# Optimization experiments

Hardware: AMD Instinct MI355X
Metric: run time of the kernel (lower is better)

The kernel has to match this reference:

```python
import jax, jax.numpy as jnp
import numpy as np

B, N, D, E = 2, 50000, 128, 640000


def setup_inputs() -> dict:
    key = jax.random.key(0)
    ks = jax.random.split(key, 7)
    x = jax.random.normal(ks[0], (B, N, D), dtype=jnp.float32)
    edge_index = jax.random.randint(ks[1], (2, E), 0, N)
    edge_attr = jax.random.uniform(ks[2], (E,), dtype=jnp.float32)
    s = 1.0 / np.sqrt(D)
    W1 = jax.random.uniform(ks[3], (D, D), jnp.float32, -s, s)
    b1 = jax.random.uniform(ks[4], (D,), jnp.float32, -s, s)
    W2 = jax.random.uniform(ks[5], (D, D), jnp.float32, -s, s)
    b2 = jax.random.uniform(ks[6], (D,), jnp.float32, -s, s)
    return {"x": x, "edge_index": edge_index, "edge_attr": edge_attr,
            "W1": W1, "b1": b1, "W2": W2, "b2": b2}


def _gcn_layer(x, W, b, row, col, norm, n):
    # x: [B, N, D] -> transform then gather-scale-scatter along edges
    h = jnp.einsum('bnd,df->bnf', x, W)
    msg = h[:, row, :] * norm[None, :, None]          # [B, E2, D]
    agg = jax.vmap(lambda m: jax.ops.segment_sum(m, col, num_segments=n))(msg)
    return agg + b


def reference(x, edge_index, edge_attr, W1, b1, W2, b2):
    n = x.shape[1]
    row, col = edge_index[0], edge_index[1]
    # GCNConv default: add self loops (weight 1), symmetric normalization
    loop = jnp.arange(n)
    row2 = jnp.concatenate([row, loop])
    col2 = jnp.concatenate([col, loop])
    w2 = jnp.concatenate([edge_attr, jnp.ones((n,), edge_attr.dtype)])
    deg = jax.ops.segment_sum(w2, col2, num_segments=n)
    dinv = jnp.where(deg > 0, jax.lax.rsqrt(deg), 0.0)
    norm = dinv[row2] * w2 * dinv[col2]               # [E2]
    # dropout is identity in eval mode
    h = jax.nn.relu(_gcn_layer(x, W1, b1, row2, col2, norm, n))
    h = jax.nn.relu(_gcn_layer(h, W2, b2, row2, col2, norm, n))
    return h
```

## Files before the change

### kernel.cpp

```cpp
#include <hip/hip_runtime.h>

#define NNODES 50000
#define NBATCH 2
#define DIM    128
#define NEDGE  640000
#define M_TOT  (NBATCH*NNODES)
#define NXCD   8
#define NBL_N  196

typedef unsigned short u16;
typedef unsigned int   u32;
typedef unsigned long long u64;

typedef __attribute__((ext_vector_type(8))) short bf16x8;
typedef __attribute__((ext_vector_type(4))) float f32x4;

__device__ __forceinline__ float bf2f(u16 u){ return __uint_as_float(((u32)u)<<16); }
__device__ __forceinline__ u16 f2bf(float f){
    u32 x = __float_as_uint(f);
    x += 0x7fffu + ((x>>16)&1u);
    return (u16)(x>>16);
}

__global__ __launch_bounds__(256) void count_k(const int* __restrict__ ei,
                                               const float* __restrict__ ea,
                                               u64* __restrict__ part,
                                               u32* __restrict__ rankpack){
    u32 xcc = __builtin_amdgcn_s_getreg(6164) & 7u;
    int e = blockIdx.x*256 + threadIdx.x;
    if (e < NEDGE){
        int c = ei[NEDGE + e];
        u64 inc = (((u64)__float2uint_rn(ea[e] * 16777216.0f)) << 32) | 1ull;
        u64 old = __hip_atomic_fetch_add(&part[(size_t)xcc*NNODES + c], inc,
                                         __ATOMIC_RELAXED, __HIP_MEMORY_SCOPE_WORKGROUP);
        rankpack[e] = ((u32)old & 0xffffu) | (xcc << 16);
    }
}

__global__ __launch_bounds__(256) void scan1(const u64* __restrict__ part,
                                             int* __restrict__ cnt,
                                             int* __restrict__ poff,
                                             float* __restrict__ dinv,
                                             int* colstart, int* bsum){
    __shared__ int s[256];
    int tid = threadIdx.x;
    int n = blockIdx.x*256 + tid;
    int v = 0;
    if (n < NNODES){
        int run = 0; u64 fsum = 0;
        #pragma unroll
        for (int p = 0; p < NXCD; ++p){
            u64 pv = part[(size_t)p*NNODES + n];
            poff[p*NNODES + n] = run;
            run  += (int)(pv & 0xffffffffu);
            fsum += (pv >> 32);
        }
        cnt[n] = run;
        v = run;
        float deg = 1.0f + (float)fsum * (1.0f/16777216.0f);
        dinv[n] = rsqrtf(deg);
    }
    s[tid] = v; __syncthreads();
    #pragma unroll
    for (int off = 1; off < 256; off <<= 1){
        int t = (tid >= off) ? s[tid-off] : 0;
        __syncthreads();
        s[tid] += t;
        __syncthreads();
    }
    if (n < NNODES) colstart[n] = s[tid] - v;
    if (tid == 255) bsum[blockIdx.x] = s[255];
}

__global__ __launch_bounds__(256) void fill_k(const int* __restrict__ ei,
                                              const float* __restrict__ ea,
                                              const float* __restrict__ dinv,
                                              const int* __restrict__ colstart,
                                              const int* __restrict__ bsum,
                                              const int* __restrict__ poff,
                                              const u32* __restrict__ rankpack,
                                              int* __restrict__ colstartF,
                                              u32* __restrict__ epk){
    __shared__ int s[256];
    __shared__ int pre[256];
    int tid = threadIdx.x;
    int v = (tid < NBL_N) ? bsum[tid] : 0;
    s[tid] = v; __syncthreads();
    #pragma unroll
    for (int off = 1; off < 256; off <<= 1){
        int t = (tid >= off) ? s[tid-off] : 0;
        __syncthreads();
        s[tid] += t;
        __syncthreads();
    }
    pre[tid] = s[tid] - v;
    __syncthreads();

    int e = blockIdx.x*256 + tid;
    if (e < NEDGE){
        int r = ei[e], c = ei[NEDGE + e];
        u32 rp = rankpack[e];
        int base = colstart[c] + pre[c >> 8];
        colstartF[c] = base;
        int pos = base + poff[(rp >> 16)*NNODES + c] + (int)(rp & 0xffffu);
        float w = dinv[r] * ea[e] * dinv[c];
        epk[pos] = (u32)r | ((u32)f2bf(w) << 16);
    }
}

__global__ __launch_bounds__(256) void transposeW(const float* __restrict__ W1, u16* __restrict__ Wt1,
                                                  const float* __restrict__ W2, u16* __restrict__ Wt2,
                                                  u64* __restrict__ part){
    int i = blockIdx.x*256 + threadIdx.x;
    const float* W = (i < 16384) ? W1 : W2;
    u16* Wt       = (i < 16384) ? Wt1 : Wt2;
    int ii = i & 16383;
    int k = ii >> 7, n = ii & 127;
    Wt[n*DIM + k] = f2bf(W[ii]);
    for (int z = i; z < NXCD*NNODES; z += 32768) part[z] = 0;
}

__device__ __forceinline__ bf16x8 load_frag(const float* A, size_t off){
    const float4* ap = (const float4*)(A + off);
    float4 lo = ap[0], hi = ap[1];
    bf16x8 r;
    r[0] = (short)f2bf(lo.x); r[1] = (short)f2bf(lo.y);
    r[2] = (short)f2bf(lo.z); r[3] = (short)f2bf(lo.w);
    r[4] = (short)f2bf(hi.x); r[5] = (short)f2bf(hi.y);
    r[6] = (short)f2bf(hi.z); r[7] = (short)f2bf(hi.w);
    return r;
}
__device__ __forceinline__ bf16x8 load_frag(const u16* A, size_t off){
    return *(const bf16x8*)(A + off);
}

template <typename AT, bool PERM>
__global__ __launch_bounds__(256) void gemm128(const AT* __restrict__ A,
                                               const u16* __restrict__ Wt,
                                               u16* __restrict__ H, int M){
    __shared__ u16 Wl[128][136];
    int tid = threadIdx.x;
    {
        const uint4* src = (const uint4*)Wt;
        #pragma unroll
        for (int j = 0; j < 8; ++j){
            int g = tid + j*256;
            int n = g >> 4;
            int k = (g & 15) * 8;
            *(uint4*)&Wl[n][k] = src[g];
        }
    }
    __syncthreads();

    int wave = tid >> 6, lane = tid & 63;
    int quad = lane >> 4, r = lane & 15;
    int row0 = blockIdx.x*256 + wave*64;

    f32x4 acc[4][8];
    #pragma unroll
    for (int mt = 0; mt < 4; ++mt)
        #pragma unroll
        for (int nt = 0; nt < 8; ++nt)
            acc[mt][nt] = (f32x4){0.f,0.f,0.f,0.f};

    #pragma unroll
    for (int ks = 0; ks < 4; ++ks){
        bf16x8 af[4];
        #pragma unroll
        for (int mt = 0; mt < 4; ++mt){
            int row = row0 + mt*16 + r;
            if (row < M)
                af[mt] = load_frag(A, (size_t)row*DIM + ks*32 + quad*8);
            else
                af[mt] = (bf16x8){0,0,0,0,0,0,0,0};
        }
        #pragma unroll
        for (int nt = 0; nt < 8; ++nt){
            bf16x8 bfr = *(const bf16x8*)&Wl[nt*16 + r][ks*32 + quad*8];
            #pragma unroll
            for (int mt = 0; mt < 4; ++mt)
                acc[mt][nt] = __builtin_amdgcn_mfma_f32_16x16x32_bf16(af[mt], bfr, acc[mt][nt], 0, 0, 0);
        }
    }

    #pragma unroll
    for (int mt = 0; mt < 4; ++mt){
        #pragma unroll
        for (int reg = 0; reg < 4; ++reg){
            int row = row0 + mt*16 + quad*4 + reg;
            if (row < M){
                size_t hrow;
                if (PERM){
                    int b = (row >= NNODES);
                    int n = row - b*NNODES;
                    hrow = (size_t)(2*n + b);
                } else {
                    hrow = (size_t)row;
                }
                #pragma unroll
                for (int nt = 0; nt < 8; ++nt)
                    H[hrow*DIM + nt*16 + r] = f2bf(acc[mt][nt][reg]);
            }
        }
    }
}

template <bool OUT_F32>
__global__ __launch_bounds__(256) void gather6_k(const u16* __restrict__ Hi,
                                                 const u32* __restrict__ epk,
                                                 const int* __restrict__ colstartF,
                                                 const int* __restrict__ cnt,
                                                 const float* __restrict__ dinv,
                                                 const float* __restrict__ bias,
                                                 void* __restrict__ out){
    int wave = threadIdx.x >> 6, lane = threadIdx.x & 63;
    int n = blockIdx.x*4 + wave;
    if (n >= NNODES) return;
    const char* Hb = (const char*)Hi;

    float a0, a1, a2, a3;
    {
        uint2 sv = *(const uint2*)(Hb + (size_t)n*512 + lane*8);
        float dn = dinv[n], dn2 = dn*dn;
        a0 = dn2*__uint_as_float(sv.x << 16);
        a1 = dn2*__uint_as_float(sv.x & 0xffff0000u);
        a2 = dn2*__uint_as_float(sv.y << 16);
        a3 = dn2*__uint_as_float(sv.y & 0xffff0000u);
    }

    int s = colstartF[n], c = cnt[n];
    for (int base = 0; base < c; base += 64){
        int m = min(64, c - base);
        u32 em = 0;
        if (lane < m) em = epk[s + base + lane];
        for (int j = 0; j < m; j += 8){
            #pragma unroll
            for (int g = 0; g < 8; ++g){
                u32 me = __shfl(em, j + g);
                uint2 v = *(const uint2*)(Hb + (size_t)(me & 0xffffu)*512 + lane*8);
                float w = __uint_as_float(me & 0xffff0000u);
                a0 = fmaf(w, __uint_as_float(v.x << 16), a0);
                a1 = fmaf(w, __uint_as_float(v.x & 0xffff0000u), a1);
                a2 = fmaf(w, __uint_as_float(v.y << 16), a2);
                a3 = fmaf(w, __uint_as_float(v.y & 0xffff0000u), a3);
            }
        }
    }

    int sub = lane & 31, b = lane >> 5;
    float4 bb = ((const float4*)bias)[sub];
    a0 = fmaxf(a0 + bb.x, 0.f);
    a1 = fmaxf(a1 + bb.y, 0.f);
    a2 = fmaxf(a2 + bb.z, 0.f);
    a3 = fmaxf(a3 + bb.w, 0.f);
    if (OUT_F32){
        float* O = (float*)out + ((size_t)b*NNODES + n)*DIM + sub*4;
        *(float4*)O = make_float4(a0, a1, a2, a3);
    } else {
        char* O = (char*)out + (size_t)n*512 + lane*8;
        uint2 pk;
        pk.x = (u32)f2bf(a0) | ((u32)f2bf(a1) << 16);
        pk.y = (u32)f2bf(a2) | ((u32)f2bf(a3) << 16);
        *(uint2*)O = pk;
    }
}

extern "C" void kernel_launch(void* const* d_in, const int* in_sizes, int n_in,
                              void* d_out, int out_size, void* d_ws, size_t ws_size,
                              hipStream_t stream){
    const float* x  = (const float*)d_in[0];
    const int*   ei = (const int*)  d_in[1];
    const float* ea = (const float*)d_in[2];
    const float* W1 = (const float*)d_in[3];
    const float* b1 = (const float*)d_in[4];
    const float* W2 = (const float*)d_in[5];
    const float* b2 = (const float*)d_in[6];

    char* p = (char*)d_ws;
    auto alloc = [&](size_t bytes)->char*{ char* r = p; p += (bytes + 511) & ~(size_t)511; return r; };
    u64*   part     = (u64*)  alloc((size_t)NXCD*NNODES*8);
    u32*   rankpack = (u32*)  alloc((size_t)NEDGE*4);
    int*   poff     = (int*)  alloc((size_t)NXCD*NNODES*4);
    float* dinv     = (float*)alloc(NNODES*4);
    int*   cnt      = (int*)  alloc(NNODES*4);
    int*   colstart = (int*)  alloc(NNODES*4);
    int*   colstartF= (int*)  alloc(NNODES*4);
    int*   bsum     = (int*)  alloc(1024);
    u32*   epk      = (u32*)  alloc((size_t)NEDGE*4);
    u16*   Wt1      = (u16*)  alloc(DIM*DIM*2);
    u16*   Wt2      = (u16*)  alloc(DIM*DIM*2);
    u16*   h        = (u16*)  alloc((size_t)M_TOT*DIM*2);
    u16*   o1       = (u16*)  alloc((size_t)M_TOT*DIM*2);

    const int NBL_E = (NEDGE  + 255)/256;
    const int NTILE = (M_TOT + 255)/256;
    const int NBL_G = (NNODES + 3)/4;

    transposeW<<<128, 256, 0, stream>>>(W1, Wt1, W2, Wt2, part);
    count_k<<<NBL_E, 256, 0, stream>>>(ei, ea, part, rankpack);
    scan1  <<<NBL_N, 256, 0, stream>>>(part, cnt, poff, dinv, colstart, bsum);
    fill_k <<<NBL_E, 256, 0, stream>>>(ei, ea, dinv, colstart, bsum, poff, rankpack, colstartF, epk);

    gemm128<float, true ><<<NTILE, 256, 0, stream>>>(x,  Wt1, h, M_TOT);
    gather6_k<false><<<NBL_G, 256, 0, stream>>>(h,  epk, colstartF, cnt, dinv, b1, o1);
    gemm128<u16,   false><<<NTILE, 256, 0, stream>>>(o1, Wt2, h, M_TOT);
    gather6_k<true ><<<NBL_G, 256, 0, stream>>>(h,  epk, colstartF, cnt, dinv, b2, d_out);
}
```

Measured before the change: 283.5 us.

## Fuse first GEMM with edge counting kernel and vectorize transposed GEMM stores

Merges the layer-1 GEMM and the edge-count atomic kernel into one launch, with the block index choosing the role, so the atomic pass can overlap the compute-bound GEMM and one launch is removed. The GEMM also swaps MFMA operand roles so each lane holds four consecutive output columns, which allows packed 8-byte stores in place of scalar 2-byte stores. Mixing the two block types may change occupancy, since GEMM blocks reserve LDS that count blocks never use.

```diff
diff --git a/kernel.cpp b/kernel.cpp
--- a/kernel.cpp
+++ b/kernel.cpp
@@ -7,6 +7,8 @@
 #define M_TOT  (NBATCH*NNODES)
 #define NXCD   8
 #define NBL_N  196
+#define NTILE  391
+#define NBL_E  2500
 
 typedef unsigned short u16;
 typedef unsigned int   u32;
@@ -22,12 +24,111 @@
     return (u16)(x>>16);
 }
 
-__global__ __launch_bounds__(256) void count_k(const int* __restrict__ ei,
-                                               const float* __restrict__ ea,
-                                               u64* __restrict__ part,
-                                               u32* __restrict__ rankpack){
+__global__ __launch_bounds__(256) void transposeW(const float* __restrict__ W1, u16* __restrict__ Wt1,
+                                                  const float* __restrict__ W2, u16* __restrict__ Wt2,
+                                                  u64* __restrict__ part){
+    int i = blockIdx.x*256 + threadIdx.x;
+    const float* W = (i < 16384) ? W1 : W2;
+    u16* Wt       = (i < 16384) ? Wt1 : Wt2;
+    int ii = i & 16383;
+    int k = ii >> 7, n = ii & 127;
+    Wt[n*DIM + k] = f2bf(W[ii]);
+    for (int z = i; z < NXCD*NNODES; z += 32768) part[z] = 0;
+}
+
+__device__ __forceinline__ bf16x8 load_frag(const float* A, size_t off){
+    const float4* ap = (const float4*)(A + off);
+    float4 lo = ap[0], hi = ap[1];
+    bf16x8 r;
+    r[0] = (short)f2bf(lo.x); r[1] = (short)f2bf(lo.y);
+    r[2] = (short)f2bf(lo.z); r[3] = (short)f2bf(lo.w);
+    r[4] = (short)f2bf(hi.x); r[5] = (short)f2bf(hi.y);
+    r[6] = (short)f2bf(hi.z); r[7] = (short)f2bf(hi.w);
+    return r;
+}
+__device__ __forceinline__ bf16x8 load_frag(const u16* A, size_t off){
+    return *(const bf16x8*)(A + off);
+}
+
+template <typename AT, bool PERM>
+__device__ __forceinline__ void gemm_body(const AT* __restrict__ A,
+                                          const u16* __restrict__ Wt,
+                                          u16* __restrict__ H, int M, int bid){
+    __shared__ u16 Wl[128][136];
+    int tid = threadIdx.x;
+    {
+        const uint4* src = (const uint4*)Wt;
+        #pragma unroll
+        for (int j = 0; j < 8; ++j){
+            int g = tid + j*256;
+            int n = g >> 4;
+            int k = (g & 15) * 8;
+            *(uint4*)&Wl[n][k] = src[g];
+        }
+    }
+    __syncthreads();
+
+    int wave = tid >> 6, lane = tid & 63;
+    int quad = lane >> 4, r = lane & 15;
+    int row0 = bid*256 + wave*64;
+
+    f32x4 acc[4][8];
+    #pragma unroll
+    for (int rt = 0; rt < 4; ++rt)
+        #pragma unroll
+        for (int mt = 0; mt < 8; ++mt)
+            acc[rt][mt] = (f32x4){0.f,0.f,0.f,0.f};
+
+    #pragma unroll
+    for (int ks = 0; ks < 4; ++ks){
+        bf16x8 bfr[4];
+        #pragma unroll
+        for (int rt = 0; rt < 4; ++rt){
+            int row = row0 + rt*16 + r;
+            if (row < M)
+                bfr[rt] = load_frag(A, (size_t)row*DIM + ks*32 + quad*8);
+            else
+                bfr[rt] = (bf16x8){0,0,0,0,0,0,0,0};
+        }
+        #pragma unroll
+        for (int mt = 0; mt < 8; ++mt){
+            bf16x8 af = *(const bf16x8*)&Wl[mt*16 + r][ks*32 + quad*8];
+            #pragma unroll
+            for (int rt = 0; rt < 4; ++rt)
+                acc[rt][mt] = __builtin_amdgcn_mfma_f32_16x16x32_bf16(af, bfr[rt], acc[rt][mt], 0, 0, 0);
+        }
+    }
+
+    #pragma unroll
+    for (int rt = 0; rt < 4; ++rt){
+        int row = row0 + rt*16 + r;
+        if (row < M){
+            size_t hrow;
+            if (PERM){
+                int b = (row >= NNODES);
+                int n = row - (b ? NNODES : 0);
+                hrow = (size_t)(2*n + b);
+            } else {
+                hrow = (size_t)row;
+            }
+            u16* Hrow = H + hrow*DIM + quad*4;
+            #pragma unroll
+            for (int mt = 0; mt < 8; ++mt){
+                uint2 pk;
+                pk.x = (u32)f2bf(acc[rt][mt][0]) | ((u32)f2bf(acc[rt][mt][1]) << 16);
+                pk.y = (u32)f2bf(acc[rt][mt][2]) | ((u32)f2bf(acc[rt][mt][3]) << 16);
+                *(uint2*)(Hrow + mt*16) = pk;
+            }
+        }
+    }
+}
+
+__device__ __forceinline__ void count_body(const int* __restrict__ ei,
+                                           const float* __restrict__ ea,
+                                           u64* __restrict__ part,
+                                           u32* __restrict__ rankpack, int bid){
     u32 xcc = __builtin_amdgcn_s_getreg(6164) & 7u;
-    int e = blockIdx.x*256 + threadIdx.x;
+    int e = bid*256 + threadIdx.x;
     if (e < NEDGE){
         int c = ei[NEDGE + e];
         u64 inc = (((u64)__float2uint_rn(ea[e] * 16777216.0f)) << 32) | 1ull;
@@ -35,6 +136,25 @@
                                          __ATOMIC_RELAXED, __HIP_MEMORY_SCOPE_WORKGROUP);
         rankpack[e] = ((u32)old & 0xffffu) | (xcc << 16);
     }
+}
+
+__global__ __launch_bounds__(256) void gemm1_count_k(const float* __restrict__ x,
+                                                     const u16* __restrict__ Wt1,
+                                                     u16* __restrict__ h,
+                                                     const int* __restrict__ ei,
+                                                     const float* __restrict__ ea,
+                                                     u64* __restrict__ part,
+                                                     u32* __restrict__ rankpack){
+    if (blockIdx.x < NTILE)
+        gemm_body<float, true>(x, Wt1, h, M_TOT, blockIdx.x);
+    else
+        count_body(ei, ea, part, rankpack, blockIdx.x - NTILE);
+}
+
+__global__ __launch_bounds__(256) void gemm2_k(const u16* __restrict__ o1,
+                                               const u16* __restrict__ Wt2,
+                                               u16* __restrict__ h){
+    gemm_body<u16, false>(o1, Wt2, h, M_TOT, blockIdx.x);
 }
 
 __global__ __launch_bounds__(256) void scan1(const u64* __restrict__ part,
@@ -105,103 +225,6 @@
         int pos = base + poff[(rp >> 16)*NNODES + c] + (int)(rp & 0xffffu);
         float w = dinv[r] * ea[e] * dinv[c];
         epk[pos] = (u32)r | ((u32)f2bf(w) << 16);
-    }
-}
-
-__global__ __launch_bounds__(256) void transposeW(const float* __restrict__ W1, u16* __restrict__ Wt1,
-                                                  const float* __restrict__ W2, u16* __restrict__ Wt2,
-                                                  u64* __restrict__ part){
-    int i = blockIdx.x*256 + threadIdx.x;
-    const float* W = (i < 16384) ? W1 : W2;
-    u16* Wt       = (i < 16384) ? Wt1 : Wt2;
-    int ii = i & 16383;
-    int k = ii >> 7, n = ii & 127;
-    Wt[n*DIM + k] = f2bf(W[ii]);
-    for (int z = i; z < NXCD*NNODES; z += 32768) part[z] = 0;
-}
-
-__device__ __forceinline__ bf16x8 load_frag(const float* A, size_t off){
-    const float4* ap = (const float4*)(A + off);
-    float4 lo = ap[0], hi = ap[1];
-    bf16x8 r;
-    r[0] = (short)f2bf(lo.x); r[1] = (short)f2bf(lo.y);
-    r[2] = (short)f2bf(lo.z); r[3] = (short)f2bf(lo.w);
-    r[4] = (short)f2bf(hi.x); r[5] = (short)f2bf(hi.y);
-    r[6] = (short)f2bf(hi.z); r[7] = (short)f2bf(hi.w);
-    return r;
-}
-__device__ __forceinline__ bf16x8 load_frag(const u16* A, size_t off){
-    return *(const bf16x8*)(A + off);
-}
-
-template <typename AT, bool PERM>
-__global__ __launch_bounds__(256) void gemm128(const AT* __restrict__ A,
-                                               const u16* __restrict__ Wt,
-                                               u16* __restrict__ H, int M){
-    __shared__ u16 Wl[128][136];
-    int tid = threadIdx.x;
-    {
-        const uint4* src = (const uint4*)Wt;
-        #pragma unroll
-        for (int j = 0; j < 8; ++j){
-            int g = tid + j*256;
-            int n = g >> 4;
-            int k = (g & 15) * 8;
-            *(uint4*)&Wl[n][k] = src[g];
-        }
-    }
-    __syncthreads();
-
-    int wave = tid >> 6, lane = tid & 63;
-    int quad = lane >> 4, r = lane & 15;
-    int row0 = blockIdx.x*256 + wave*64;
-
-    f32x4 acc[4][8];
-    #pragma unroll
-    for (int mt = 0; mt < 4; ++mt)
-        #pragma unroll
-        for (int nt = 0; nt < 8; ++nt)
-            acc[mt][nt] = (f32x4){0.f,0.f,0.f,0.f};
-
-    #pragma unroll
-    for (int ks = 0; ks < 4; ++ks){
-        bf16x8 af[4];
-        #pragma unroll
-        for (int mt = 0; mt < 4; ++mt){
-            int row = row0 + mt*16 + r;
-            if (row < M)
-                af[mt] = load_frag(A, (size_t)row*DIM + ks*32 + quad*8);
-            else
-                af[mt] = (bf16x8){0,0,0,0,0,0,0,0};
-        }
-        #pragma unroll
-        for (int nt = 0; nt < 8; ++nt){
-            bf16x8 bfr = *(const bf16x8*)&Wl[nt*16 + r][ks*32 + quad*8];
-            #pragma unroll
-            for (int mt = 0; mt < 4; ++mt)
-                acc[mt][nt] = __builtin_amdgcn_mfma_f32_16x16x32_bf16(af[mt], bfr, acc[mt][nt], 0, 0, 0);
-        }
-    }
-
-    #pragma unroll
-    for (int mt = 0; mt < 4; ++mt){
-        #pragma unroll
-        for (int reg = 0; reg < 4; ++reg){
-            int row = row0 + mt*16 + quad*4 + reg;
-            if (row < M){
-                size_t hrow;
-                if (PERM){
-                    int b = (row >= NNODES);
-                    int n = row - b*NNODES;
-                    hrow = (size_t)(2*n + b);
-                } else {
-                    hrow = (size_t)row;
-                }
-                #pragma unroll
-                for (int nt = 0; nt < 8; ++nt)
-                    H[hrow*DIM + nt*16 + r] = f2bf(acc[mt][nt][reg]);
-            }
-        }
     }
 }
 
@@ -292,17 +315,14 @@
     u16*   h        = (u16*)  alloc((size_t)M_TOT*DIM*2);
     u16*   o1       = (u16*)  alloc((size_t)M_TOT*DIM*2);
 
-    const int NBL_E = (NEDGE  + 255)/256;
-    const int NTILE = (M_TOT + 255)/256;
     const int NBL_G = (NNODES + 3)/4;
 
     transposeW<<<128, 256, 0, stream>>>(W1, Wt1, W2, Wt2, part);
-    count_k<<<NBL_E, 256, 0, stream>>>(ei, ea, part, rankpack);
-    scan1  <<<NBL_N, 256, 0, stream>>>(part, cnt, poff, dinv, colstart, bsum);
-    fill_k <<<NBL_E, 256, 0, stream>>>(ei, ea, dinv, colstart, bsum, poff, rankpack, colstartF, epk);
-
-    gemm128<float, true ><<<NTILE, 256, 0, stream>>>(x,  Wt1, h, M_TOT);
-    gather6_k<false><<<NBL_G, 256, 0, stream>>>(h,  epk, colstartF, cnt, dinv, b1, o1);
-    gemm128<u16,   false><<<NTILE, 256, 0, stream>>>(o1, Wt2, h, M_TOT);
-    gather6_k<true ><<<NBL_G, 256, 0, stream>>>(h,  epk, colstartF, cnt, dinv, b2, d_out);
-}
+    gemm1_count_k<<<NTILE + NBL_E, 256, 0, stream>>>(x, Wt1, h, ei, ea, part, rankpack);
+    scan1 <<<NBL_N, 256, 0, stream>>>(part, cnt, poff, dinv, colstart, bsum);
+    fill_k<<<NBL_E, 256, 0, stream>>>(ei, ea, dinv, colstart, bsum, poff, rankpack, colstartF, epk);
+
+    gather6_k<false><<<NBL_G, 256, 0, stream>>>(h, epk, colstartF, cnt, dinv, b1, o1);
+    gemm2_k<<<NTILE, 256, 0, stream>>>(o1, Wt2, h);
+    gather6_k<true ><<<NBL_G, 256, 0, stream>>>(h, epk, colstartF, cnt, dinv, b2, d_out);
+}
```

Measured after the change: 287.9 us. No clear change (+1.6%).
